# Kernel tuning notes

Measured on AMD Instinct MI355X. Metric: run time of the kernel, lower is better.

The kernel has to match this reference:

```python
import jax, jax.numpy as jnp
import numpy as np

B, Q, MEM, U, H = 2, 1024, 1024, 1024, 16
DH = U // H
KLEN = MEM + Q


def setup_inputs() -> dict:
    key = jax.random.key(0)
    ks = jax.random.split(key, 9)
    return {
        "inputs": jax.random.normal(ks[0], (B, Q, U), jnp.float32),
        "relatives": jax.random.normal(ks[1], (B, KLEN, U), jnp.float32),
        "memories": jax.random.normal(ks[2], (B, MEM, U), jnp.float32),
        "bias_context": jax.random.normal(ks[3], (U,), jnp.float32) * 0.02,
        "bias_relative": jax.random.normal(ks[4], (U,), jnp.float32) * 0.02,
        "Wq": jax.random.normal(ks[5], (U, U), jnp.float32) * 0.02,
        "Wkv": jax.random.normal(ks[6], (U, 2 * U), jnp.float32) * 0.02,
        "Wr": jax.random.normal(ks[7], (U, U), jnp.float32) * 0.02,
        "Wo": jax.random.normal(ks[8], (U, U), jnp.float32) * 0.02,
    }


def _split_heads(x):
    # (B, L, U) -> (B, L, H, DH)
    b, l, _ = x.shape
    return x.reshape(b, l, H, DH)


def _relative_shift(x):
    # x: (B, H, q, k) -> Transformer-XL pad/reshape/slice shift
    b, h, q, k = x.shape
    x = jnp.pad(x, ((0, 0), (0, 0), (0, 0), (1, 0)))
    x = x.reshape(b, h, k + 1, q)
    x = x[:, :, 1:, :]
    return x.reshape(b, h, q, k)


def reference(inputs, relatives, memories, bias_context, bias_relative, Wq, Wkv, Wr, Wo):
    full = jnp.concatenate([memories, inputs], axis=1)  # (B, KLEN, U)
    w_q = inputs @ Wq                                    # (B, Q, U)
    w_kv = full @ Wkv                                    # (B, KLEN, 2U)
    w_r = relatives @ Wr                                 # (B, KLEN, U)
    w_k, w_v = w_kv[..., :U], w_kv[..., U:]

    qc = _split_heads(w_q + bias_context)                # (B, Q, H, DH)
    qr = _split_heads(w_q + bias_relative)
    k = _split_heads(w_k)                                # (B, KLEN, H, DH)
    v = _split_heads(w_v)
    r = _split_heads(w_r)

    a_context = jnp.einsum("bqhd,bkhd->bhqk", qc, k)
    a_relative = _relative_shift(jnp.einsum("bqhd,bkhd->bhqk", qr, r))
    att = (a_context + a_relative) / jnp.sqrt(jnp.asarray(DH, att_dtype := a_context.dtype))

    # causal mask: key index j visible to query i iff j <= (KLEN - Q) + i
    idx = jnp.arange(KLEN)[None, :]
    upper = jnp.arange(KLEN - Q, KLEN)[:, None]
    mask = idx <= upper                                  # (Q, KLEN)
    att = jnp.where(mask[None, None], att, jnp.asarray(-jnp.inf, att_dtype))
    att = jax.nn.softmax(att, axis=-1)                   # (B, H, Q, KLEN)

    out = jnp.einsum("bhqk,bkhd->bqhd", att, v).reshape(B, Q, U)
    return out @ Wo
```

## Files before the change

### kernel.cpp

```cpp
#include <hip/hip_runtime.h>
#include <math.h>
#include <stdint.h>

using u16 = unsigned short;
using u32 = uint32_t;

constexpr int cB = 2;
constexpr int cQ = 1024;
constexpr int cM = 1024;
constexpr int cU = 1024;
constexpr int cH = 16;
constexpr int cD = 64;
constexpr int cK = 2048;
constexpr int cRROWS = 2112;
constexpr int cWPAD = 2176;

typedef __bf16 v8bf  __attribute__((ext_vector_type(8)));
typedef float  v16f  __attribute__((ext_vector_type(16)));

#define MFMA32(a, b, c) __builtin_amdgcn_mfma_f32_32x32x16_bf16((a), (b), (c), 0, 0, 0)

__device__ __forceinline__ u16 f2bf(float f) {
    u32 u = __float_as_uint(f);
    u += 0x7fffu + ((u >> 16) & 1u);
    return (u16)(u >> 16);
}
__device__ __forceinline__ float bf2f(u16 s) {
    return __uint_as_float(((u32)s) << 16);
}

union Frag { v8bf v; u16 s[8]; uint2 d2[2]; uint4 q4; };

typedef const u32 __attribute__((address_space(1)))* gp1;
typedef u32 __attribute__((address_space(3)))* lp3;

__global__ __launch_bounds__(256)
void convert_acts(const float* __restrict__ inputs, const float* __restrict__ memories,
                  const float* __restrict__ relatives,
                  u16* __restrict__ fullH, u16* __restrict__ fullL,
                  u16* __restrict__ relH,  u16* __restrict__ relL)
{
    const int idx = blockIdx.x * 256 + threadIdx.x;
    const float* src;
    u16 *dh, *dl;
    int q;
    if (idx < (1 << 20)) {
        q = idx;
        const int row = q >> 8;
        const int col = (q & 255) * 4;
        const int b = row >> 11, l = row & (cK - 1);
        src = (l < cM) ? (memories + ((size_t)b * cM + l) * cU + col)
                       : (inputs   + ((size_t)b * cQ + (l - cM)) * cU + col);
        dh = fullH; dl = fullL;
    } else {
        q = idx - (1 << 20);
        src = relatives + (size_t)q * 4;
        dh = relH; dl = relL;
    }
    const float4 f = *(const float4*)src;
    const float xs[4] = {f.x, f.y, f.z, f.w};
    u16 hi[4], lo[4];
    #pragma unroll
    for (int j = 0; j < 4; ++j) {
        hi[j] = f2bf(xs[j]);
        lo[j] = f2bf(xs[j] - bf2f(hi[j]));
    }
    uint2 ph, pl;
    ph.x = hi[0] | ((u32)hi[1] << 16); ph.y = hi[2] | ((u32)hi[3] << 16);
    pl.x = lo[0] | ((u32)lo[1] << 16); pl.y = lo[2] | ((u32)lo[3] << 16);
    *(uint2*)(dh + (size_t)q * 4) = ph;
    *(uint2*)(dl + (size_t)q * 4) = pl;
}

__global__ __launch_bounds__(256)
void convert_wT(const float* __restrict__ Wq, const float* __restrict__ Wkv,
                const float* __restrict__ Wr, const float* __restrict__ Wo,
                u16* __restrict__ WqTH, u16* __restrict__ WqTL,
                u16* __restrict__ WkvTH, u16* __restrict__ WkvTL,
                u16* __restrict__ WrTH, u16* __restrict__ WrTL,
                u16* __restrict__ WoTH, u16* __restrict__ WoTL)
{
    __shared__ float tl[64][65];
    const int t = threadIdx.x;
    int bid = blockIdx.x;
    const float* src; u16 *dh, *dl; int N, tK, tN;
    if (bid < 256)       { src = Wq;  dh = WqTH;  dl = WqTL;  N = 1024; tK = bid >> 4; tN = bid & 15; }
    else if (bid < 768)  { bid -= 256; src = Wkv; dh = WkvTH; dl = WkvTL; N = 2048; tK = bid >> 5; tN = bid & 31; }
    else if (bid < 1024) { bid -= 768; src = Wr;  dh = WrTH;  dl = WrTL;  N = 1024; tK = bid >> 4; tN = bid & 15; }
    else                 { bid -= 1024; src = Wo; dh = WoTH;  dl = WoTL;  N = 1024; tK = bid >> 4; tN = bid & 15; }
    const int k0 = tK * 64, n0 = tN * 64;

    #pragma unroll
    for (int i = 0; i < 16; ++i) {
        const int idx = i * 256 + t;
        const int r = idx >> 6, c = idx & 63;
        tl[r][c] = src[(size_t)(k0 + r) * N + n0 + c];
    }
    __syncthreads();
    #pragma unroll
    for (int i = 0; i < 16; ++i) {
        const int idx = i * 256 + t;
        const int rn = idx >> 6, ck = idx & 63;
        const float x = tl[ck][rn];
        const u16 hi = f2bf(x);
        const u16 lo = f2bf(x - bf2f(hi));
        const size_t o = (size_t)(n0 + rn) * 1024 + k0 + ck;
        dh[o] = hi; dl[o] = lo;
    }
}

__global__ __launch_bounds__(256)
void gemm_mfma(const u16* __restrict__ fullH, const u16* __restrict__ fullL,
               const u16* __restrict__ relH,  const u16* __restrict__ relL,
               const u16* __restrict__ WqTH,  const u16* __restrict__ WqTL,
               const u16* __restrict__ WkvTH, const u16* __restrict__ WkvTL,
               const u16* __restrict__ WrTH,  const u16* __restrict__ WrTL,
               const u16* __restrict__ atH,   const u16* __restrict__ atL,
               const u16* __restrict__ WoTH,  const u16* __restrict__ WoTL,
               const float* __restrict__ bias_c,
               float* __restrict__ qc, u16* __restrict__ kb16, u16* __restrict__ vb16,
               u16* __restrict__ rb16, float* __restrict__ outp, int base)
{
    __shared__ uint4 ldsbuf[2048];
    char* lds = (char*)ldsbuf;

    int bid = blockIdx.x;
    int mode, m0, n0, arow0, npass;
    const u16 *aH, *aL, *bH, *bL;
    if (base == 4) {
        const int x = bid & 7, g = bid >> 3;
        m0 = ((x >> 1) * 4 + (g >> 2)) * 128;
        n0 = ((x & 1) * 4 + (g & 3)) * 128;
        mode = 4; aH = atH; aL = atL; bH = WoTH; bL = WoTL; arow0 = m0; npass = 3;
    } else if (bid < 128) {
        const int x = bid & 7, g = bid >> 3;
        m0 = ((x >> 1) * 4 + (g >> 2)) * 128;
        n0 = ((x & 1) * 4 + (g & 3)) * 128;
        mode = 1; aH = fullH; aL = fullL; bH = WqTH; bL = WqTL;
        arow0 = (m0 >> 10) * cK + cM + (m0 & (cQ - 1)); npass = 2;
    } else if (bid < 640) {
        const int local = bid - 128;
        const int x = local & 7, g = local >> 3;
        m0 = ((x >> 1) * 8 + (g >> 3)) * 128;
        n0 = ((x & 1) * 8 + (g & 7)) * 128;
        mode = 2; aH = fullH; aL = fullL; bH = WkvTH; bL = WkvTL; arow0 = m0;
        npass = (n0 >= cU) ? 1 : 2;
    } else {
        const int local = bid - 640;
        const int x = local & 7, g = local >> 3;
        m0 = ((x >> 1) * 8 + (g >> 2)) * 128;
        n0 = ((x & 1) * 4 + (g & 3)) * 128;
        mode = 3; aH = relH; aL = relL; bH = WrTH; bL = WrTL; arow0 = m0; npass = 2;
    }

    const int t = threadIdx.x, w = t >> 6, lane = t & 63;

    const int rl = lane >> 2;
    const int cl = (lane & 3) ^ ((lane >> 3) & 3);
    const u16* src;
    if (w == 0)      src = aH + (size_t)(arow0 + rl) * 1024 + cl * 8;
    else if (w == 1) src = aL + (size_t)(arow0 + rl) * 1024 + cl * 8;
    else if (w == 2) src = bH + (size_t)(n0 + rl) * 1024 + cl * 8;
    else             src = bL + (size_t)(n0 + rl) * 1024 + cl * 8;
    char* ldsw = lds + w * 8192;
    const bool doStage = (w == 0) || (w == 2) || (w == 1 && npass >= 2) || (w == 3 && npass >= 3);

    const int l31 = lane & 31, hk = lane >> 5;
    const int fsw = (l31 >> 1) & 3;
    const int koff[2] = { ((hk ^ fsw) << 4), (((2 + hk) ^ fsw) << 4) };
    const int mwb = (w >> 1) * 4096 + l31 * 64;
    const int nwb = (w & 1) * 4096 + l31 * 64;

    v16f acc[2][2];
    #pragma unroll
    for (int i = 0; i < 16; ++i) { acc[0][0][i] = 0.f; acc[0][1][i] = 0.f; acc[1][0][i] = 0.f; acc[1][1][i] = 0.f; }

    for (int kit = 0; kit < 32; ++kit) {
        __syncthreads();
        if (doStage) {
            #pragma unroll
            for (int g2 = 0; g2 < 8; ++g2)
                __builtin_amdgcn_global_load_lds((gp1)(src + (size_t)g2 * 16 * 1024),
                                                 (lp3)(ldsw + g2 * 1024), 16, 0, 0);
        }
        src += 32;
        __syncthreads();

        #pragma unroll
        for (int s = 0; s < 2; ++s) {
            const int ko = koff[s];
            const v8bf ah0 = *(const v8bf*)(lds + mwb + ko);
            const v8bf ah1 = *(const v8bf*)(lds + mwb + 2048 + ko);
            const v8bf bh0 = *(const v8bf*)(lds + 16384 + nwb + ko);
            const v8bf bh1 = *(const v8bf*)(lds + 16384 + nwb + 2048 + ko);
            acc[0][0] = MFMA32(ah0, bh0, acc[0][0]);
            acc[0][1] = MFMA32(ah0, bh1, acc[0][1]);
            acc[1][0] = MFMA32(ah1, bh0, acc[1][0]);
            acc[1][1] = MFMA32(ah1, bh1, acc[1][1]);
            if (npass >= 2) {
                const v8bf al0 = *(const v8bf*)(lds + 8192 + mwb + ko);
                const v8bf al1 = *(const v8bf*)(lds + 8192 + mwb + 2048 + ko);
                acc[0][0] = MFMA32(al0, bh0, acc[0][0]);
                acc[0][1] = MFMA32(al0, bh1, acc[0][1]);
                acc[1][0] = MFMA32(al1, bh0, acc[1][0]);
                acc[1][1] = MFMA32(al1, bh1, acc[1][1]);
            }
            if (npass >= 3) {
                const v8bf bl0 = *(const v8bf*)(lds + 24576 + nwb + ko);
                const v8bf bl1 = *(const v8bf*)(lds + 24576 + nwb + 2048 + ko);
                acc[0][0] = MFMA32(ah0, bl0, acc[0][0]);
                acc[0][1] = MFMA32(ah0, bl1, acc[0][1]);
                acc[1][0] = MFMA32(ah1, bl0, acc[1][0]);
                acc[1][1] = MFMA32(ah1, bl1, acc[1][1]);
            }
        }
    }

    #pragma unroll
    for (int mi = 0; mi < 2; ++mi)
    #pragma unroll
    for (int ni = 0; ni < 2; ++ni) {
        const int n = n0 + (w & 1) * 64 + ni * 32 + l31;
        #pragma unroll
        for (int e = 0; e < 16; ++e) {
            const int m = m0 + (w >> 1) * 64 + mi * 32 + (e & 3) + 8 * (e >> 2) + 4 * hk;
            const float v = acc[mi][ni][e];
            if (mode == 1) {
                const int b = m >> 10, q = m & (cQ - 1);
                const int h = n >> 6, d = n & 63;
                qc[(((size_t)(b * cH + h)) * cQ + q) * cD + d] = v + bias_c[n];
            } else if (mode == 2) {
                const int b = m >> 11, l = m & (cK - 1);
                const int nn = n & (cU - 1);
                const int h = nn >> 6, d = nn & 63;
                if (n >= cU)
                    vb16[(size_t)(b * cH + h) * cK * cD + ((l >> 6) * 4096)
                         + (((l >> 4) & 3) * 1024) + (((l >> 3) & 1) * 512)
                         + d * 8 + (l & 7)] = f2bf(v);
                else
                    kb16[(size_t)(b * cH + h) * cK * cD + ((l >> 6) * 4096)
                         + ((d >> 4) * 1024) + (((d >> 3) & 1) * 512)
                         + ((l & 63) * 8) + (d & 7)] = f2bf(v);
            } else if (mode == 3) {
                const int b = m >> 11, l = m & (cK - 1);
                const int h = n >> 6, d = n & 63;
                rb16[(size_t)(b * cH + h) * cRROWS * cD + ((l >> 5) * 2048)
                     + ((d >> 4) * 512) + (((d >> 3) & 1) * 256)
                     + ((l & 31) * 8) + (d & 7)] = f2bf(v);
            } else {
                outp[(size_t)m * cU + n] = v;
            }
        }
    }
}

__global__ __launch_bounds__(256)
void wvec_kernel(const u16* __restrict__ rb16, const float* __restrict__ bias_c,
                 const float* __restrict__ bias_r, float* __restrict__ w_all)
{
    const int t = threadIdx.x, w = t >> 6, lane = t & 63;
    #pragma unroll 4
    for (int it = 0; it < 16; ++it) {
        const int row = blockIdx.x * 64 + it * 4 + w;
        const int bh = row >> 11, g = row & (cK - 1);
        const int h = bh & (cH - 1);
        const float d = bias_r[h * 64 + lane] - bias_c[h * 64 + lane];
        const size_t idx = (size_t)bh * cRROWS * cD + ((g >> 5) * 2048)
                         + ((lane >> 4) * 512) + (((lane >> 3) & 1) * 256)
                         + ((g & 31) * 8) + (lane & 7);
        float v = bf2f(rb16[idx]) * d;
        #pragma unroll
        for (int off = 1; off <= 32; off <<= 1)
            v += __shfl_xor(v, off);
        if (lane == 0) w_all[(size_t)bh * cWPAD + g] = v;
    }
}

__global__ __launch_bounds__(256, 4)
void flash_mfma(const float* __restrict__ qcg, const u16* __restrict__ kbg,
                const u16* __restrict__ vbg, const u16* __restrict__ rbg,
                const float* __restrict__ w_all,
                float* __restrict__ oPart, float* __restrict__ lPart)
{
    __shared__ u16 KhL[4096];
    __shared__ u16 RhL[8192];
    __shared__ u16 SrelT[128][68];
    __shared__ u16 Ph[64][68];
    __shared__ float lrow[2][64];

    const int bid = blockIdx.x;
    const int hb = bid & 31;
    const int inner = bid >> 5;
    const int qb = inner & 15;
    const int sp = inner >> 4;
    const int h = hb >> 1, b = hb & 1;
    const int bh = b * cH + h;
    const int q0 = qb * 64;

    const u16* kgf = kbg + (size_t)bh * cK * cD;
    const u16* vgf = vbg + (size_t)bh * cK * cD;
    const u16* rgf = rbg + (size_t)bh * cRROWS * cD;
    const float* qg = qcg + (size_t)bh * cQ * cD;
    const float* wg = w_all + (size_t)bh * cWPAD;

    const int t = threadIdx.x, w = t >> 6, lane = t & 63;
    const int l31 = lane & 31, hk = lane >> 5;
    const int rloc0 = (w >> 1) * 32;
    const int c0 = (w & 1) * 32;
    const int wc0 = (w & 1) * 64 + l31;

    Frag qch[4];
    {
        const float* qrow = qg + (size_t)(q0 + rloc0 + l31) * cD;
        #pragma unroll
        for (int kc = 0; kc < 4; ++kc) {
            const int dh0 = kc * 16 + hk * 8;
            const float4 f0 = *(const float4*)(qrow + dh0);
            const float4 f1 = *(const float4*)(qrow + dh0 + 4);
            const float xs[8] = {f0.x, f0.y, f0.z, f0.w, f1.x, f1.y, f1.z, f1.w};
            #pragma unroll
            for (int j = 0; j < 8; ++j) qch[kc].s[j] = f2bf(xs[j]);
        }
    }

    v16f aO;
    float lpart[16];
    #pragma unroll
    for (int i = 0; i < 16; ++i) { aO[i] = 0.f; lpart[i] = 0.f; }

    const int nch = 17 + qb;
    int j0 = sp * 64;

    auto dma = [&](int jn, int relbn) {
        #pragma unroll
        for (int i = 0; i < 6; ++i) {
            const int id = w * 6 + i;
            if (id < 8) {
                const u16* s = kgf + (size_t)(jn >> 6) * 4096 + id * 512;
                __builtin_amdgcn_global_load_lds((gp1)(s + lane * 8),
                                                 (lp3)((char*)KhL + id * 1024), 16, 0, 0);
            } else {
                const int jj = id - 8;
                const u16* s = rgf + ((size_t)(relbn >> 5) + (jj >> 2)) * 2048 + (jj & 3) * 512;
                __builtin_amdgcn_global_load_lds((gp1)(s + lane * 8),
                                                 (lp3)((char*)RhL + jj * 1024), 16, 0, 0);
            }
        }
    };

    dma(j0, j0 - q0 + 960);
    __syncthreads();

    for (int c = sp; c < nch; c += 2) {
        const int relbase = j0 - q0 + 960;

        Frag vf[4];
        #pragma unroll
        for (int kc = 0; kc < 4; ++kc)
            vf[kc].q4 = *(const uint4*)(vgf + (size_t)(j0 >> 6) * 4096
                                        + kc * 1024 + hk * 512 + (c0 + l31) * 8);
        const float wv0 = wg[relbase + wc0];
        const float wv1 = wg[relbase + wc0 + 32];

        v16f actx;
        #pragma unroll
        for (int i = 0; i < 16; ++i) actx[i] = 0.f;
        #pragma unroll
        for (int kc = 0; kc < 4; ++kc) {
            Frag kf;
            kf.q4 = *(const uint4*)(KhL + kc * 1024 + hk * 512 + (c0 + l31) * 8);
            actx = MFMA32(qch[kc].v, kf.v, actx);
        }

        #pragma unroll
        for (int half = 0; half < 2; ++half) {
            v16f ar;
            #pragma unroll
            for (int i = 0; i < 16; ++i) ar[i] = 0.f;
            const int lg = (w & 1) * 2 + half;
            #pragma unroll
            for (int kc = 0; kc < 4; ++kc) {
                Frag rf;
                rf.q4 = *(const uint4*)(RhL + lg * 2048 + kc * 512 + hk * 256 + l31 * 8);
                ar = MFMA32(qch[kc].v, rf.v, ar);
            }
            const float wvh = half ? wv1 : wv0;
            const int wch = wc0 + half * 32;
            #pragma unroll
            for (int g = 0; g < 4; ++g) {
                const int rb_ = rloc0 + 8 * g + 4 * hk;
                u16 p[4];
                #pragma unroll
                for (int e = 0; e < 4; ++e) p[e] = f2bf(ar[4 * g + e] + wvh);
                *(uint2*)&SrelT[wch][rb_] = make_uint2(p[0] | ((u32)p[1] << 16),
                                                       p[2] | ((u32)p[3] << 16));
            }
        }
        __syncthreads();

        const int jn = (c + 2 < nch) ? j0 + 128 : j0;
        dma(jn, jn - q0 + 960);

        const int jl = c0 + l31;
        const int limit = cM + q0 - j0;
        #pragma unroll
        for (int g = 0; g < 4; ++g)
        #pragma unroll
        for (int e = 0; e < 4; ++e) {
            const int reg  = 4 * g + e;
            const int rloc = rloc0 + e + 8 * g + 4 * hk;
            const int widx = jl - rloc + 63;
            const float srel = bf2f(SrelT[widx][rloc]);
            const float s = (actx[reg] + srel) * 0.125f - 10.f;
            const float p = (jl > limit + rloc) ? 0.f : __expf(s);
            lpart[reg] += p;
            Ph[rloc][jl] = f2bf(p);
        }
        __syncthreads();

        #pragma unroll
        for (int kc = 0; kc < 4; ++kc) {
            const int kb0 = kc * 16 + hk * 8;
            Frag pf;
            pf.d2[0] = *(const uint2*)&Ph[rloc0 + l31][kb0];
            pf.d2[1] = *(const uint2*)&Ph[rloc0 + l31][kb0 + 4];
            aO = MFMA32(pf.v, vf[kc].v, aO);
        }
        j0 += 128;
    }

    #pragma unroll
    for (int off = 1; off <= 16; off <<= 1)
        #pragma unroll
        for (int i = 0; i < 16; ++i) lpart[i] += __shfl_xor(lpart[i], off);
    if (l31 == 0) {
        #pragma unroll
        for (int g = 0; g < 4; ++g)
        #pragma unroll
        for (int e = 0; e < 4; ++e)
            lrow[w & 1][rloc0 + e + 8 * g + 4 * hk] = lpart[4 * g + e];
    }
    __syncthreads();

    float* ob = oPart + (size_t)sp * ((size_t)cB * cQ * cU);
    #pragma unroll
    for (int g = 0; g < 4; ++g)
    #pragma unroll
    for (int e = 0; e < 4; ++e) {
        const int reg  = 4 * g + e;
        const int rloc = rloc0 + e + 8 * g + 4 * hk;
        ob[((size_t)(b * cQ + q0 + rloc)) * cU + h * 64 + c0 + l31] = aO[reg];
    }
    if (t < 64)
        lPart[(size_t)sp * (cB * cH * cQ) + (size_t)bh * cQ + q0 + t] = lrow[0][t] + lrow[1][t];
}

__global__ __launch_bounds__(256)
void combine(const float* __restrict__ oPart, const float* __restrict__ lPart,
             u16* __restrict__ atH, u16* __restrict__ atL)
{
    const int idx = blockIdx.x * 256 + threadIdx.x;
    const size_t base = (size_t)idx * 4;
    const int b = (int)(base >> 20);
    const int rem = (int)(base & ((1u << 20) - 1));
    const int q = rem >> 10;
    const int u = rem & 1023;
    const int h = u >> 6;
    const float4 o0 = *(const float4*)(oPart + base);
    const float4 o1 = *(const float4*)(oPart + (size_t)cB * cQ * cU + base);
    const int li = (b * cH + h) * cQ + q;
    const float l = lPart[li] + lPart[cB * cH * cQ + li];
    const float inv = 1.f / l;
    const float vals[4] = {(o0.x + o1.x) * inv, (o0.y + o1.y) * inv,
                           (o0.z + o1.z) * inv, (o0.w + o1.w) * inv};
    u16 hi[4], lo[4];
    #pragma unroll
    for (int j = 0; j < 4; ++j) {
        hi[j] = f2bf(vals[j]);
        lo[j] = f2bf(vals[j] - bf2f(hi[j]));
    }
    uint2 ph, pl;
    ph.x = hi[0] | ((u32)hi[1] << 16); ph.y = hi[2] | ((u32)hi[3] << 16);
    pl.x = lo[0] | ((u32)lo[1] << 16); pl.y = lo[2] | ((u32)lo[3] << 16);
    *(uint2*)(atH + base) = ph;
    *(uint2*)(atL + base) = pl;
}

extern "C" void kernel_launch(void* const* d_in, const int* in_sizes, int n_in,
                              void* d_out, int out_size, void* d_ws, size_t ws_size,
                              hipStream_t stream)
{
    const float* inputs    = (const float*)d_in[0];
    const float* relatives = (const float*)d_in[1];
    const float* memories  = (const float*)d_in[2];
    const float* bias_c    = (const float*)d_in[3];
    const float* bias_r    = (const float*)d_in[4];
    const float* Wq        = (const float*)d_in[5];
    const float* Wkv       = (const float*)d_in[6];
    const float* Wr        = (const float*)d_in[7];
    const float* Wo        = (const float*)d_in[8];
    float* out = (float*)d_out;

    char* p = (char*)d_ws;
    auto alloc = [&](size_t bytes) { char* r = p; p += bytes; return r; };
    u16* fullH = (u16*)alloc(8u << 20);
    u16* fullL = (u16*)alloc(8u << 20);
    u16* relH  = (u16*)alloc(8u << 20);
    u16* relL  = (u16*)alloc(8u << 20);
    u16* WqTH  = (u16*)alloc(2u << 20);
    u16* WqTL  = (u16*)alloc(2u << 20);
    u16* WkvTH = (u16*)alloc(4u << 20);
    u16* WkvTL = (u16*)alloc(4u << 20);
    u16* WrTH  = (u16*)alloc(2u << 20);
    u16* WrTL  = (u16*)alloc(2u << 20);
    u16* WoTH  = (u16*)alloc(2u << 20);
    u16* WoTL  = (u16*)alloc(2u << 20);
    float* qc  = (float*)alloc(8u << 20);
    u16* kb16  = (u16*)alloc(8u << 20);
    u16* vb16  = (u16*)alloc(8u << 20);
    u16* rb16  = (u16*)alloc(9u << 20);
    float* w_all = (float*)alloc(32u * cWPAD * 4u);
    float* lPart = (float*)alloc(2u * cB * cH * cQ * 4u);
    u16* atH   = (u16*)alloc(4u << 20);
    u16* atL   = (u16*)alloc(4u << 20);
    float* oPart = (float*)relH;

    convert_acts<<<8192, 256, 0, stream>>>(inputs, memories, relatives,
                                           fullH, fullL, relH, relL);
    convert_wT<<<1280, 256, 0, stream>>>(Wq, Wkv, Wr, Wo,
                                         WqTH, WqTL, WkvTH, WkvTL,
                                         WrTH, WrTL, WoTH, WoTL);
    gemm_mfma<<<896, 256, 0, stream>>>(fullH, fullL, relH, relL,
                                       WqTH, WqTL, WkvTH, WkvTL, WrTH, WrTL,
                                       atH, atL, WoTH, WoTL, bias_c,
                                       qc, kb16, vb16, rb16, out, 0);
    wvec_kernel<<<1024, 256, 0, stream>>>(rb16, bias_c, bias_r, w_all);
    flash_mfma<<<1024, 256, 0, stream>>>(qc, kb16, vb16, rb16, w_all, oPart, lPart);
    combine<<<2048, 256, 0, stream>>>(oPart, lPart, atH, atL);
    gemm_mfma<<<128, 256, 0, stream>>>(fullH, fullL, relH, relL,
                                       WqTH, WqTL, WkvTH, WkvTL, WrTH, WrTL,
                                       atH, atL, WoTH, WoTL, bias_c,
                                       qc, kb16, vb16, rb16, out, 4);
}
```

Before: 332.1 us.

## Double-buffer LDS staging in split-bf16 GEMM with async prefetch two steps ahead

```diff
diff --git a/kernel.cpp b/kernel.cpp
--- a/kernel.cpp
+++ b/kernel.cpp
@@ -121,8 +121,7 @@
                float* __restrict__ qc, u16* __restrict__ kb16, u16* __restrict__ vb16,
                u16* __restrict__ rb16, float* __restrict__ outp, int base)
 {
-    __shared__ uint4 ldsbuf[2048];
-    char* lds = (char*)ldsbuf;
+    extern __shared__ char lds[];
 
     int bid = blockIdx.x;
     int mode, m0, n0, arow0, npass;
@@ -153,6 +152,8 @@
         mode = 3; aH = relH; aL = relL; bH = WrTH; bL = WrTL; arow0 = m0; npass = 2;
     }
 
+    const int BSTR = (base == 4) ? 32768 : 24576;
+
     const int t = threadIdx.x, w = t >> 6, lane = t & 63;
 
     const int rl = lane >> 2;
@@ -162,8 +163,19 @@
     else if (w == 1) src = aL + (size_t)(arow0 + rl) * 1024 + cl * 8;
     else if (w == 2) src = bH + (size_t)(n0 + rl) * 1024 + cl * 8;
     else             src = bL + (size_t)(n0 + rl) * 1024 + cl * 8;
-    char* ldsw = lds + w * 8192;
+    const int planeOff = w * 8192;
     const bool doStage = (w == 0) || (w == 2) || (w == 1 && npass >= 2) || (w == 3 && npass >= 3);
+
+    auto stage = [&](int k, int buf) {
+        if (doStage) {
+            const u16* s = src + (size_t)k * 32;
+            char* dst = lds + buf * BSTR + planeOff;
+            #pragma unroll
+            for (int g2 = 0; g2 < 8; ++g2)
+                __builtin_amdgcn_global_load_lds((gp1)(s + (size_t)g2 * 16 * 1024),
+                                                 (lp3)(dst + g2 * 1024), 16, 0, 0);
+        }
+    };
 
     const int l31 = lane & 31, hk = lane >> 5;
     const int fsw = (l31 >> 1) & 3;
@@ -175,45 +187,59 @@
     #pragma unroll
     for (int i = 0; i < 16; ++i) { acc[0][0][i] = 0.f; acc[0][1][i] = 0.f; acc[1][0][i] = 0.f; acc[1][1][i] = 0.f; }
 
+    stage(0, 0);
+    stage(1, 1);
+    asm volatile("s_waitcnt vmcnt(8)" ::: "memory");
+    __builtin_amdgcn_s_barrier();
+    asm volatile("" ::: "memory");
+
     for (int kit = 0; kit < 32; ++kit) {
-        __syncthreads();
-        if (doStage) {
-            #pragma unroll
-            for (int g2 = 0; g2 < 8; ++g2)
-                __builtin_amdgcn_global_load_lds((gp1)(src + (size_t)g2 * 16 * 1024),
-                                                 (lp3)(ldsw + g2 * 1024), 16, 0, 0);
-        }
-        src += 32;
-        __syncthreads();
+        const char* ldsb = lds + ((kit & 1) ? BSTR : 0);
 
         #pragma unroll
         for (int s = 0; s < 2; ++s) {
             const int ko = koff[s];
-            const v8bf ah0 = *(const v8bf*)(lds + mwb + ko);
-            const v8bf ah1 = *(const v8bf*)(lds + mwb + 2048 + ko);
-            const v8bf bh0 = *(const v8bf*)(lds + 16384 + nwb + ko);
-            const v8bf bh1 = *(const v8bf*)(lds + 16384 + nwb + 2048 + ko);
+            const v8bf ah0 = *(const v8bf*)(ldsb + mwb + ko);
+            const v8bf ah1 = *(const v8bf*)(ldsb + mwb + 2048 + ko);
+            const v8bf bh0 = *(const v8bf*)(ldsb + 16384 + nwb + ko);
+            const v8bf bh1 = *(const v8bf*)(ldsb + 16384 + nwb + 2048 + ko);
             acc[0][0] = MFMA32(ah0, bh0, acc[0][0]);
             acc[0][1] = MFMA32(ah0, bh1, acc[0][1]);
             acc[1][0] = MFMA32(ah1, bh0, acc[1][0]);
             acc[1][1] = MFMA32(ah1, bh1, acc[1][1]);
             if (npass >= 2) {
-                const v8bf al0 = *(const v8bf*)(lds + 8192 + mwb + ko);
-                const v8bf al1 = *(const v8bf*)(lds + 8192 + mwb + 2048 + ko);
+                const v8bf al0 = *(const v8bf*)(ldsb + 8192 + mwb + ko);
+                const v8bf al1 = *(const v8bf*)(ldsb + 8192 + mwb + 2048 + ko);
                 acc[0][0] = MFMA32(al0, bh0, acc[0][0]);
                 acc[0][1] = MFMA32(al0, bh1, acc[0][1]);
                 acc[1][0] = MFMA32(al1, bh0, acc[1][0]);
                 acc[1][1] = MFMA32(al1, bh1, acc[1][1]);
             }
             if (npass >= 3) {
-                const v8bf bl0 = *(const v8bf*)(lds + 24576 + nwb + ko);
-                const v8bf bl1 = *(const v8bf*)(lds + 24576 + nwb + 2048 + ko);
+                const v8bf bl0 = *(const v8bf*)(ldsb + 24576 + nwb + ko);
+                const v8bf bl1 = *(const v8bf*)(ldsb + 24576 + nwb + 2048 + ko);
                 acc[0][0] = MFMA32(ah0, bl0, acc[0][0]);
                 acc[0][1] = MFMA32(ah0, bl1, acc[0][1]);
                 acc[1][0] = MFMA32(ah1, bl0, acc[1][0]);
                 acc[1][1] = MFMA32(ah1, bl1, acc[1][1]);
             }
         }
+
+        if (kit == 31) break;
+
+        asm volatile("" ::: "memory");
+        __builtin_amdgcn_s_barrier();
+        asm volatile("" ::: "memory");
+
+        if (kit <= 29) {
+            stage(kit + 2, kit & 1);
+            asm volatile("s_waitcnt vmcnt(8)" ::: "memory");
+        } else {
+            asm volatile("s_waitcnt vmcnt(0)" ::: "memory");
+        }
+
+        __builtin_amdgcn_s_barrier();
+        asm volatile("" ::: "memory");
     }
 
     #pragma unroll
@@ -530,15 +556,15 @@
     convert_wT<<<1280, 256, 0, stream>>>(Wq, Wkv, Wr, Wo,
                                          WqTH, WqTL, WkvTH, WkvTL,
                                          WrTH, WrTL, WoTH, WoTL);
-    gemm_mfma<<<896, 256, 0, stream>>>(fullH, fullL, relH, relL,
-                                       WqTH, WqTL, WkvTH, WkvTL, WrTH, WrTL,
-                                       atH, atL, WoTH, WoTL, bias_c,
-                                       qc, kb16, vb16, rb16, out, 0);
+    gemm_mfma<<<896, 256, 49152, stream>>>(fullH, fullL, relH, relL,
+                                           WqTH, WqTL, WkvTH, WkvTL, WrTH, WrTL,
+                                           atH, atL, WoTH, WoTL, bias_c,
+                                           qc, kb16, vb16, rb16, out, 0);
     wvec_kernel<<<1024, 256, 0, stream>>>(rb16, bias_c, bias_r, w_all);
     flash_mfma<<<1024, 256, 0, stream>>>(qc, kb16, vb16, rb16, w_all, oPart, lPart);
     combine<<<2048, 256, 0, stream>>>(oPart, lPart, atH, atL);
-    gemm_mfma<<<128, 256, 0, stream>>>(fullH, fullL, relH, relL,
-                                       WqTH, WqTL, WkvTH, WkvTL, WrTH, WrTL,
-                                       atH, atL, WoTH, WoTL, bias_c,
-                                       qc, kb16, vb16, rb16, out, 4);
-}
+    gemm_mfma<<<128, 256, 65536, stream>>>(fullH, fullL, relH, relL,
+                                           WqTH, WqTL, WkvTH, WkvTL, WrTH, WrTL,
+                                           atH, atL, WoTH, WoTL, bias_c,
+                                           qc, kb16, vb16, rb16, out, 4);
+}
```

After: 311.3 us. 1.07x faster.
